# Kernel optimization log

Measured on AMD Instinct MI355X. Metric: run time of the kernel, lower is better.

The kernel has to match this reference:

```python
import jax, jax.numpy as jnp
import numpy as np
from jax import lax

DH = 256   # d_hidden
NL = 8     # number of wavenet cells
K = 3      # kernel_size
DIN = 16   # d_lag + d_cov
DOUT = 1
T, B = 1024, 64


def setup_inputs() -> dict:
    key = jax.random.key(0)
    ks = jax.random.split(key, 20)
    s = 0.05
    inp = {
        "X_emb": jax.random.randint(ks[0], (T, B, 1), 0, 10),
        "X_cov": jax.random.normal(ks[1], (T, B, 8), jnp.float32),
        "X_lag": jax.random.normal(ks[2], (T, B, 8), jnp.float32),
        "y": jax.random.normal(ks[3], (T, B, DOUT), jnp.float32),
        "domain": jax.random.uniform(ks[4], (B, 4), jnp.float32),
        "up_w": jax.random.normal(ks[5], (DIN, DH), jnp.float32) * s,
        "up_b": jnp.zeros((DH,), jnp.float32),
        "conv_dil_w": jax.random.normal(ks[6], (NL, 2 * DH, DH, K), jnp.float32) * s,
        "conv_dil_b": jnp.zeros((NL, 2 * DH), jnp.float32),
        "skip_w": jax.random.normal(ks[7], (NL, 2 * DH, DH), jnp.float32) * s,
        "skip_b": jnp.zeros((NL, 2 * DH), jnp.float32),
        "fc_w": jax.random.normal(ks[8], (DH, DH), jnp.float32) * s,
        "fc_b": jnp.zeros((DH,), jnp.float32),
        "loc_w": jax.random.normal(ks[9], (DH, DOUT), jnp.float32) * s,
        "loc_b": jnp.zeros((DOUT,), jnp.float32),
        "scale_w": jax.random.normal(ks[10], (DH, DOUT), jnp.float32) * s,
        "scale_b": jnp.zeros((DOUT,), jnp.float32),
        "d_outputseqlen": 24,
    }
    return inp


def _causal_conv(h, w, b, dil):
    # h: [B, C, T], w: [O, C, K] -> causal (left-padded) dilated conv
    pad = (w.shape[-1] - 1) * dil
    y = lax.conv_general_dilated(h, w, window_strides=(1,), padding=[(pad, 0)],
                                 rhs_dilation=(dil,),
                                 dimension_numbers=("NCH", "OIH", "NCH"))
    return y + b[None, :, None]


def _forward(X_cov, X_lag, y, up_w, up_b, conv_dil_w, conv_dil_b,
             skip_w, skip_b, fc_w, fc_b, loc_w, loc_b, scale_w, scale_b,
             d_outputseqlen):
    t = X_lag.shape[0]
    h = jnp.concatenate([X_lag, X_cov[:t]], axis=-1) @ up_w + up_b  # [T,B,DH]
    h = jnp.transpose(h, (1, 2, 0))  # [B, DH, T]
    skip = jnp.zeros_like(h)
    for i in range(NL):
        fg = _causal_conv(h, conv_dil_w[i], conv_dil_b[i], 2 ** i)  # [B,2DH,T]
        f, g = jnp.split(fg, 2, axis=1)
        gated = jnp.tanh(f) * jax.nn.sigmoid(g)  # [B,DH,T]
        hs = jnp.einsum("oc,bct->bot", skip_w[i], gated) + skip_b[i][None, :, None]
        h_next, skip_next = jnp.split(hs, 2, axis=1)
        h = h + h_next
        skip = skip + skip_next
    feat = jnp.transpose(skip, (2, 0, 1))  # [T,B,DH]
    ff = jax.nn.relu(feat @ fc_w + fc_b)
    tail = ff[-d_outputseqlen:]
    loc = tail @ loc_w + loc_b
    scale = jax.nn.softplus(tail @ scale_w + scale_b) + 1e-6
    yt = y[-d_outputseqlen:]
    log_prob = (-0.5 * ((yt - loc) / scale) ** 2
                - jnp.log(scale) - 0.5 * np.log(2.0 * np.pi))
    loss_y = -jnp.mean(log_prob)
    total_loss = loss_y  # loss_d forced to 0 in the original forward
    return total_loss, loss_y, loc, scale


def reference(X_emb, X_cov, X_lag, y, domain, up_w, up_b, conv_dil_w,
              conv_dil_b, skip_w, skip_b, fc_w, fc_b, loc_w, loc_b,
              scale_w, scale_b, d_outputseqlen):
    # X_emb and domain are unused with d_emb=[] and loss_d hard-set to 0.
    return _forward(X_cov, X_lag, y, up_w, up_b, conv_dil_w, conv_dil_b,
                    skip_w, skip_b, fc_w, fc_b, loc_w, loc_b,
                    scale_w, scale_b, d_outputseqlen)
```

## Files before the change

kernel.cpp:

```cpp
#include <hip/hip_runtime.h>
#include <math.h>

static constexpr int TT = 1024, BB = 64, DHID = 256, NLAY = 8, OSL = 24;
static constexpr int T0H = 192, THN = 832;
static constexpr int T0G = 256, TGN = 768;

typedef __attribute__((ext_vector_type(8))) short short8;
typedef __attribute__((ext_vector_type(4))) float f32x4;
typedef unsigned short u16;
typedef __attribute__((ext_vector_type(4))) unsigned short u16x4;
typedef unsigned int u32;

__device__ __forceinline__ u16 f2bf(float x) {
  u32 u = __float_as_uint(x);
  return (u16)((u + 0x7fffu + ((u >> 16) & 1u)) >> 16);
}
__device__ __forceinline__ float bf2f(u16 v) {
  return __uint_as_float((u32)v << 16);
}

__global__ __launch_bounds__(256) void wprep(
    const float* __restrict__ cw, const float* __restrict__ sw,
    u16* __restrict__ wP, u16* __restrict__ swH, u16* __restrict__ swG)
{
  const int stride = gridDim.x * 256;
  for (int i = blockIdx.x * 256 + threadIdx.x; i < NLAY * 3 * 8 * 2 * 4 * 2048; i += stride) {
    const int e = i & 7, row = (i >> 3) & 255;
    int q = i >> 11;
    const int p = q & 3; q >>= 2;
    const int cs = q & 1; q >>= 1;
    const int kc = q & 7; q >>= 3;
    const int tap = q % 3, l = q / 3;
    const int o = (row < 128) ? (cs * 128 + row) : (256 + cs * 128 + (row - 128));
    const int c = kc * 32 + p * 8 + e;
    wP[i] = f2bf(cw[((size_t)(l * 512 + o) * 256 + c) * 3 + tap]);
  }
  for (int i = blockIdx.x * 256 + threadIdx.x; i < NLAY * 8 * 4 * 2048; i += stride) {
    const int e = i & 7, o = (i >> 3) & 255, p = (i >> 11) & 3, kc = (i >> 13) & 7, l = i >> 16;
    const int c = kc * 32 + p * 8 + e;
    swH[i] = f2bf(sw[(size_t)(l * 512 + o) * 256 + c]);
    swG[i] = f2bf(sw[(size_t)(l * 512 + 256 + o) * 256 + c]);
  }
}

__global__ __launch_bounds__(256) void up_kernel(
    const float* __restrict__ xlag, const float* __restrict__ xcov,
    const float* __restrict__ upw, const float* __restrict__ upb,
    u16* __restrict__ hb0)
{
  const int b  = blockIdx.y;
  const int t0 = T0H + blockIdx.x * 16;
  __shared__ float xs[16][17];
  {
    const int tl = threadIdx.x >> 4;
    const int j  = threadIdx.x & 15;
    const size_t base = ((size_t)(t0 + tl) * BB + b) * 8;
    xs[tl][j] = (j < 8) ? xlag[base + j] : xcov[base + (j - 8)];
  }
  __syncthreads();
  const int c = threadIdx.x;
  float uw[16];
#pragma unroll
  for (int j = 0; j < 16; ++j) uw[j] = upw[j * DHID + c];
  const float bias = upb[c];
#pragma unroll
  for (int tl = 0; tl < 16; ++tl) {
    float acc = bias;
#pragma unroll
    for (int j = 0; j < 16; ++j) acc = fmaf(xs[tl][j], uw[j], acc);
    hb0[(((size_t)b * 32 + (c >> 3)) * THN + (t0 + tl - T0H)) * 8 + (c & 7)] = f2bf(acc);
  }
}

template <int DIL>
__global__ __launch_bounds__(1024) void conv_gate(
    const u16* __restrict__ hbin, const u16* __restrict__ wPl,
    const float* __restrict__ cb, u16* __restrict__ gbuf,
    u16* __restrict__ g15l, const int tile0)
{
  __shared__ u16 AB[2][16384];
  const int tid = threadIdx.x, w = tid >> 6, lane = tid & 63;
  const int l16 = lane & 15, quad = lane >> 4;
  const int mw = w & 3, nw = w >> 2;
  const int tile = tile0 + (int)(blockIdx.x >> 4);
  const int b0 = (blockIdx.x & 15) * 4;
  const int cs = blockIdx.y;
  const int t0 = tile * 64;

  const int ctb = tid >> 8, pb = (tid >> 6) & 3, tlb = tid & 63;

  const u16* wBase = wPl + (size_t)cs * 8192 + tid * 8;
  const u16* hBase = hbin + (((size_t)(b0 + ctb) * 32 + pb) * THN + (t0 - T0H + tlb)) * 8;

  auto loadA = [&](int step) -> short8 {
    return *(const short8*)(wBase + (size_t)step * 16384);
  };
  auto loadB = [&](int step) -> short8 {
    const int tap = step >> 3, kc = step & 7;
    const int sh = (2 - tap) * DIL;
    return *(const short8*)(hBase + ((size_t)kc * 4 * THN - sh) * 8);
  };

  f32x4 acc[4][4];
  const f32x4 zero = {0.f, 0.f, 0.f, 0.f};
#pragma unroll
  for (int m = 0; m < 4; ++m)
#pragma unroll
    for (int j = 0; j < 4; ++j) acc[m][j] = zero;

  short8 vaN, vbN, vaF, vbF;
  {
    short8 va = loadA(0);
    short8 vb = loadB(0);
    *(short8*)&AB[0][(size_t)tid * 8] = va;
    *(short8*)&AB[0][8192 + (size_t)tid * 8] = vb;
    vaN = loadA(1);
    vbN = loadB(1);
  }
  __syncthreads();

#pragma unroll
  for (int step = 0; step < 24; ++step) {
    const int n2 = step + 2;
    if (n2 < 24) {
      vaF = loadA(n2);
      vbF = loadB(n2);
    }
    const u16* A = AB[step & 1];
    const u16* B = AB[step & 1] + 8192;
    short8 bfr[4];
#pragma unroll
    for (int j = 0; j < 4; ++j)
      bfr[j] = *(const short8*)&B[(nw * 256 + quad * 64 + 16 * j + l16) * 8];
#pragma unroll
    for (int m = 0; m < 4; ++m) {
      const int row = (m < 2) ? (mw * 32 + 16 * m) : (128 + mw * 32 + 16 * (m - 2));
      const short8 a = *(const short8*)&A[(quad * 256 + row + l16) * 8];
#pragma unroll
      for (int j = 0; j < 4; ++j)
        acc[m][j] = __builtin_amdgcn_mfma_f32_16x16x32_bf16(a, bfr[j], acc[m][j], 0, 0, 0);
    }
    const int ns = step + 1;
    if (ns < 24) {
      *(short8*)&AB[ns & 1][(size_t)tid * 8] = vaN;
      *(short8*)&AB[ns & 1][8192 + (size_t)tid * 8] = vbN;
    }
    vaN = vaF; vbN = vbF;
    __syncthreads();
  }

  u16* gT = (u16*)AB;
#pragma unroll
  for (int m = 0; m < 2; ++m) {
    const int c4 = mw * 32 + 16 * m + quad * 4;
    const int cpl = c4 >> 3;
#pragma unroll
    for (int j = 0; j < 4; ++j) {
      const int tl = 16 * j + l16;
      u16x4 pk;
#pragma unroll
      for (int r = 0; r < 4; ++r) {
        const float f = acc[m][j][r]     + cb[cs * 128 + c4 + r];
        const float g = acc[m + 2][j][r] + cb[256 + cs * 128 + c4 + r];
        const float th = 2.f / (1.f + __expf(-2.f * f)) - 1.f;
        const float sg = 1.f / (1.f + __expf(-g));
        pk[r] = f2bf(th * sg);
      }
      *(u16x4*)&gT[((nw * 16 + cpl) * 64 + tl) * 8 + (quad & 1) * 4] = pk;
    }
  }
  __syncthreads();
#pragma unroll
  for (int k = 0; k < 4; ++k) {
    const int slot = k * 1024 + tid;
    const int ct = slot >> 10, cpl = (slot >> 6) & 15, tl = slot & 63;
    const short8 v = *(const short8*)&gT[slot * 8];
    const int b = b0 + ct, cpg = cs * 16 + cpl;
    *(short8*)&gbuf[(((size_t)b * 32 + cpg) * TGN + (t0 + tl - T0G)) * 8] = v;
    if (tile == 15)
      *(short8*)&g15l[(((size_t)b * 32 + cpg) * 64 + tl) * 8] = v;
  }
}

__global__ __launch_bounds__(1024) void skip_h(
    const u16* __restrict__ gbuf, const u16* __restrict__ swHl,
    const float* __restrict__ sb, const u16* __restrict__ hbin,
    u16* __restrict__ hbout, const int tile0)
{
  __shared__ u16 AB[2][16384];
  const int tid = threadIdx.x, w = tid >> 6, lane = tid & 63;
  const int l16 = lane & 15, quad = lane >> 4;
  const int mw = w & 3, nw = w >> 2;
  const int tile = tile0 + (int)(blockIdx.x >> 4);
  const int b0 = (blockIdx.x & 15) * 4;
  const int t0 = tile * 64;

  const int ctb = tid >> 8, pb = (tid >> 6) & 3, tlb = tid & 63;

  const u16* aBase = swHl + tid * 8;
  const u16* bBase = gbuf + (((size_t)(b0 + ctb) * 32 + pb) * TGN + (t0 - T0G + tlb)) * 8;

  auto loadA = [&](int kc) -> short8 {
    return *(const short8*)(aBase + (size_t)kc * 8192);
  };
  auto loadB = [&](int kc) -> short8 {
    return *(const short8*)(bBase + (size_t)kc * 4 * TGN * 8);
  };

  f32x4 acc[4][4];
  const f32x4 zero = {0.f, 0.f, 0.f, 0.f};
#pragma unroll
  for (int m = 0; m < 4; ++m)
#pragma unroll
    for (int j = 0; j < 4; ++j) acc[m][j] = zero;

  short8 vaN, vbN, vaF, vbF;
  {
    short8 va = loadA(0);
    short8 vb = loadB(0);
    *(short8*)&AB[0][(size_t)tid * 8] = va;
    *(short8*)&AB[0][8192 + (size_t)tid * 8] = vb;
    vaN = loadA(1);
    vbN = loadB(1);
  }
  __syncthreads();

#pragma unroll
  for (int step = 0; step < 8; ++step) {
    const int n2 = step + 2;
    if (n2 < 8) { vaF = loadA(n2); vbF = loadB(n2); }
    const u16* A = AB[step & 1];
    const u16* B = AB[step & 1] + 8192;
    short8 bfr[4];
#pragma unroll
    for (int j = 0; j < 4; ++j)
      bfr[j] = *(const short8*)&B[(nw * 256 + quad * 64 + 16 * j + l16) * 8];
#pragma unroll
    for (int m = 0; m < 4; ++m) {
      const short8 a = *(const short8*)&A[(quad * 256 + mw * 64 + 16 * m + l16) * 8];
#pragma unroll
      for (int j = 0; j < 4; ++j)
        acc[m][j] = __builtin_amdgcn_mfma_f32_16x16x32_bf16(a, bfr[j], acc[m][j], 0, 0, 0);
    }
    const int ns = step + 1;
    if (ns < 8) {
      *(short8*)&AB[ns & 1][(size_t)tid * 8] = vaN;
      *(short8*)&AB[ns & 1][8192 + (size_t)tid * 8] = vbN;
    }
    vaN = vaF; vbN = vbF;
    __syncthreads();
  }

  float* fT = (float*)AB;
  for (int ctr = 0; ctr < 4; ++ctr) {
    __syncthreads();
    if (nw == ctr) {
#pragma unroll
      for (int m = 0; m < 4; ++m) {
        const int c4 = mw * 64 + 16 * m + quad * 4;
#pragma unroll
        for (int j = 0; j < 4; ++j) {
          const int tl = 16 * j + l16;
          f32x4 v;
#pragma unroll
          for (int r = 0; r < 4; ++r) v[r] = acc[m][j][r] + sb[c4 + r];
          *(f32x4*)&fT[((c4 >> 3) * 64 + tl) * 8 + (quad & 1) * 4] = v;
        }
      }
    }
    __syncthreads();
    const int b = b0 + ctr;
#pragma unroll
    for (int k = 0; k < 2; ++k) {
      const int slot = k * 1024 + tid;
      const int cpl = slot >> 6, tl = slot & 63;
      const size_t idx = (((size_t)b * 32 + cpl) * THN + (t0 - T0H + tl)) * 8;
      const short8 hv = *(const short8*)&hbin[idx];
      short8 ov;
#pragma unroll
      for (int e = 0; e < 8; ++e)
        ov[e] = (short)f2bf(bf2f((u16)hv[e]) + fT[slot * 8 + e]);
      *(short8*)&hbout[idx] = ov;
    }
  }
}

__global__ __launch_bounds__(512) void skip_g(
    const u16* __restrict__ g15, const u16* __restrict__ swG,
    float* __restrict__ gpart)
{
  __shared__ u16 AB[2][9216];
  const int tid = threadIdx.x, w = tid >> 6, lane = tid & 63;
  const int l16 = lane & 15, quad = lane >> 4;
  const int b = blockIdx.x, l = blockIdx.y;

  const u16* aBase = swG + (size_t)l * 65536 + tid * 8;
  const int pB = tid >> 5, tlB = tid & 31;
  const u16* bBase = g15 + ((((size_t)l * 64 + b) * 32 + pB) * 64 + 32 + tlB) * 8;

  auto loadA = [&](int kc, int q) -> short8 {
    return *(const short8*)(aBase + (size_t)kc * 8192 + q * 4096);
  };
  auto loadB = [&](int kc) -> short8 {
    return *(const short8*)(bBase + (size_t)kc * 4 * 64 * 8);
  };

  f32x4 acc[2][2];
  const f32x4 zero = {0.f, 0.f, 0.f, 0.f};
#pragma unroll
  for (int m = 0; m < 2; ++m)
#pragma unroll
    for (int j = 0; j < 2; ++j) acc[m][j] = zero;

  short8 a0N, a1N, vbN, a0F, a1F, vbF;
  {
    short8 a0 = loadA(0, 0), a1 = loadA(0, 1);
    *(short8*)&AB[0][(size_t)tid * 8] = a0;
    *(short8*)&AB[0][(size_t)(512 + tid) * 8] = a1;
    if (tid < 128) {
      short8 vb = loadB(0);
      *(short8*)&AB[0][8192 + (size_t)tid * 8] = vb;
    }
    a0N = loadA(1, 0); a1N = loadA(1, 1);
    if (tid < 128) vbN = loadB(1);
  }
  __syncthreads();

#pragma unroll
  for (int step = 0; step < 8; ++step) {
    const int n2 = step + 2;
    if (n2 < 8) {
      a0F = loadA(n2, 0); a1F = loadA(n2, 1);
      if (tid < 128) vbF = loadB(n2);
    }
    const u16* A = AB[step & 1];
    const u16* B = AB[step & 1] + 8192;
    short8 bfr[2];
#pragma unroll
    for (int j = 0; j < 2; ++j)
      bfr[j] = *(const short8*)&B[(quad * 32 + 16 * j + l16) * 8];
#pragma unroll
    for (int m = 0; m < 2; ++m) {
      const short8 a = *(const short8*)&A[(quad * 256 + w * 32 + 16 * m + l16) * 8];
#pragma unroll
      for (int j = 0; j < 2; ++j)
        acc[m][j] = __builtin_amdgcn_mfma_f32_16x16x32_bf16(a, bfr[j], acc[m][j], 0, 0, 0);
    }
    const int ns = step + 1;
    if (ns < 8) {
      *(short8*)&AB[ns & 1][(size_t)tid * 8] = a0N;
      *(short8*)&AB[ns & 1][(size_t)(512 + tid) * 8] = a1N;
      if (tid < 128) *(short8*)&AB[ns & 1][8192 + (size_t)tid * 8] = vbN;
    }
    a0N = a0F; a1N = a1F; vbN = vbF;
    __syncthreads();
  }
#pragma unroll
  for (int m = 0; m < 2; ++m)
#pragma unroll
    for (int j = 0; j < 2; ++j)
#pragma unroll
      for (int r = 0; r < 4; ++r) {
        const int c = w * 32 + 16 * m + quad * 4 + r;
        gpart[(((size_t)l * 64 + b) * 256 + c) * 32 + 16 * j + l16] = acc[m][j][r];
      }
}

__global__ __launch_bounds__(256) void head_kernel(
    const float* __restrict__ gpart, const float* __restrict__ skip_b,
    const float* __restrict__ fcw, const float* __restrict__ fcb,
    const float* __restrict__ locw, const float* __restrict__ locb,
    const float* __restrict__ scw, const float* __restrict__ scb,
    float* __restrict__ out)
{
  const int tt = blockIdx.x;
  const int b  = blockIdx.y;
  const int c  = threadIdx.x;
  __shared__ float xs[DHID];
  float s = 0.f;
#pragma unroll
  for (int l = 0; l < NLAY; ++l) {
    s += skip_b[l * 512 + 256 + c];
    s += gpart[(((size_t)l * 64 + b) * 256 + c) * 32 + (8 + tt)];
  }
  xs[c] = s;
  __syncthreads();
  float acc = fcb[c];
#pragma unroll 8
  for (int j = 0; j < DHID; ++j) acc = fmaf(xs[j], fcw[j * DHID + c], acc);
  const float ff = fmaxf(acc, 0.f);
  float pl = ff * locw[c];
  float ps = ff * scw[c];
#pragma unroll
  for (int off = 32; off > 0; off >>= 1) {
    pl += __shfl_down(pl, off);
    ps += __shfl_down(ps, off);
  }
  __shared__ float rl[4], rs[4];
  const int wid = threadIdx.x >> 6, lane = threadIdx.x & 63;
  if (lane == 0) { rl[wid] = pl; rs[wid] = ps; }
  __syncthreads();
  if (threadIdx.x == 0) {
    const float loc = rl[0] + rl[1] + rl[2] + rl[3] + locb[0];
    const float x   = rs[0] + rs[1] + rs[2] + rs[3] + scb[0];
    const float sp  = (x > 0.f) ? (x + log1pf(expf(-x))) : log1pf(expf(x));
    out[2 + tt * BB + b]            = loc;
    out[2 + OSL * BB + tt * BB + b] = sp + 1e-6f;
  }
}

__global__ __launch_bounds__(256) void loss_kernel(
    const float* __restrict__ y, float* __restrict__ out)
{
  float s = 0.f;
  for (int i = threadIdx.x; i < OSL * BB; i += 256) {
    const int tt = i >> 6, b = i & 63;
    const float loc = out[2 + i];
    const float sc  = out[2 + OSL * BB + i];
    const float yt  = y[(size_t)(TT - OSL + tt) * BB + b];
    const float z   = (yt - loc) / sc;
    s += -0.5f * z * z - logf(sc) - 0.9189385332046727f;
  }
#pragma unroll
  for (int off = 32; off > 0; off >>= 1) s += __shfl_down(s, off);
  __shared__ float r[4];
  if ((threadIdx.x & 63) == 0) r[threadIdx.x >> 6] = s;
  __syncthreads();
  if (threadIdx.x == 0) {
    const float loss = -(r[0] + r[1] + r[2] + r[3]) / (float)(OSL * BB);
    out[0] = loss;
    out[1] = loss;
  }
}

extern "C" void kernel_launch(void* const* d_in, const int* in_sizes, int n_in,
                              void* d_out, int out_size, void* d_ws, size_t ws_size,
                              hipStream_t stream) {
  (void)in_sizes; (void)n_in; (void)out_size; (void)ws_size;
  const float* X_cov  = (const float*)d_in[1];
  const float* X_lag  = (const float*)d_in[2];
  const float* y      = (const float*)d_in[3];
  const float* up_w   = (const float*)d_in[5];
  const float* up_b   = (const float*)d_in[6];
  const float* conv_w = (const float*)d_in[7];
  const float* conv_b = (const float*)d_in[8];
  const float* skip_w = (const float*)d_in[9];
  const float* skip_b = (const float*)d_in[10];
  const float* fc_w   = (const float*)d_in[11];
  const float* fc_b   = (const float*)d_in[12];
  const float* loc_w  = (const float*)d_in[13];
  const float* loc_b  = (const float*)d_in[14];
  const float* sc_w   = (const float*)d_in[15];
  const float* sc_b   = (const float*)d_in[16];

  char* wsb = (char*)d_ws;
  u16*   hb0   = (u16*)(wsb + 0);
  u16*   hb1   = (u16*)(wsb + 27262976);
  u16*   gbuf  = (u16*)(wsb + 54525952);
  u16*   g15   = (u16*)(wsb + 79691776);
  u16*   wP    = (u16*)(wsb + 96468992);
  u16*   swH   = (u16*)(wsb + 102760448);
  u16*   swG   = (u16*)(wsb + 103809024);
  float* gpart = (float*)(wsb + 104857600);

  wprep<<<1024, 256, 0, stream>>>(conv_w, skip_w, wP, swH, swG);
  up_kernel<<<dim3(52, BB), 256, 0, stream>>>(X_lag, X_cov, up_w, up_b, hb0);

  static const int Ptab[NLAY] = {4, 5, 6, 7, 8, 9, 11, 15};
  u16* hin = hb0;
  u16* hout = hb1;
  for (int i = 0; i < NLAY; ++i) {
    const int ntiles = 16 - Ptab[i];
    const dim3 cg(ntiles * 16, 2);
    const u16* wPl = wP + (size_t)i * 393216;
    const float* cbl = conv_b + i * 512;
    u16* g15l = g15 + (size_t)i * 1048576;
    switch (i) {
      case 0: conv_gate<1>  <<<cg, 1024, 0, stream>>>(hin, wPl, cbl, gbuf, g15l, Ptab[i]); break;
      case 1: conv_gate<2>  <<<cg, 1024, 0, stream>>>(hin, wPl, cbl, gbuf, g15l, Ptab[i]); break;
      case 2: conv_gate<4>  <<<cg, 1024, 0, stream>>>(hin, wPl, cbl, gbuf, g15l, Ptab[i]); break;
      case 3: conv_gate<8>  <<<cg, 1024, 0, stream>>>(hin, wPl, cbl, gbuf, g15l, Ptab[i]); break;
      case 4: conv_gate<16> <<<cg, 1024, 0, stream>>>(hin, wPl, cbl, gbuf, g15l, Ptab[i]); break;
      case 5: conv_gate<32> <<<cg, 1024, 0, stream>>>(hin, wPl, cbl, gbuf, g15l, Ptab[i]); break;
      case 6: conv_gate<64> <<<cg, 1024, 0, stream>>>(hin, wPl, cbl, gbuf, g15l, Ptab[i]); break;
      case 7: conv_gate<128><<<cg, 1024, 0, stream>>>(hin, wPl, cbl, gbuf, g15l, Ptab[i]); break;
    }
    skip_h<<<dim3(ntiles * 16), 1024, 0, stream>>>(
        gbuf, swH + (size_t)i * 65536, skip_b + i * 512, hin, hout, Ptab[i]);
    u16* tmp = hin; hin = hout; hout = tmp;
  }

  skip_g<<<dim3(64, 8), 512, 0, stream>>>(g15, swG, gpart);
  head_kernel<<<dim3(OSL, BB), 256, 0, stream>>>(
      gpart, skip_b, fc_w, fc_b, loc_w, loc_b, sc_w, sc_b, (float*)d_out);
  loss_kernel<<<1, 256, 0, stream>>>(y, (float*)d_out);
}
```

Measured before the change: 685.4 us.

## Halve block size to 512 threads, de-template dilation, skip last layer's h update

Conv_gate and skip_h now run 512-thread blocks that each cover two batch elements instead of four, with smaller shared buffers and launch bounds asking for 4 blocks per CU. The A-operand tile is loaded as two halves per thread, and the prefetch is shortened from two steps ahead to one. The dilation becomes a runtime argument instead of a template parameter, and the main loops are no longer fully unrolled. The final layer's skip_h launch is dropped, since its h output is never read. The aim is more resident blocks and finer grids for better latency hiding and load balance, at the cost of shallower prefetch and possibly less-optimised non-unrolled loops.

```diff
diff --git a/kernel.cpp b/kernel.cpp
--- a/kernel.cpp
+++ b/kernel.cpp
@@ -72,18 +72,17 @@
   }
 }
 
-template <int DIL>
-__global__ __launch_bounds__(1024) void conv_gate(
+__global__ __launch_bounds__(512, 4) void conv_gate(
     const u16* __restrict__ hbin, const u16* __restrict__ wPl,
     const float* __restrict__ cb, u16* __restrict__ gbuf,
-    u16* __restrict__ g15l, const int tile0)
-{
-  __shared__ u16 AB[2][16384];
+    u16* __restrict__ g15l, const int dil, const int tile0)
+{
+  __shared__ u16 AB[2][12288];
   const int tid = threadIdx.x, w = tid >> 6, lane = tid & 63;
   const int l16 = lane & 15, quad = lane >> 4;
   const int mw = w & 3, nw = w >> 2;
-  const int tile = tile0 + (int)(blockIdx.x >> 4);
-  const int b0 = (blockIdx.x & 15) * 4;
+  const int tile = tile0 + (int)(blockIdx.x >> 5);
+  const int b0 = (blockIdx.x & 31) * 2;
   const int cs = blockIdx.y;
   const int t0 = tile * 64;
 
@@ -92,13 +91,16 @@
   const u16* wBase = wPl + (size_t)cs * 8192 + tid * 8;
   const u16* hBase = hbin + (((size_t)(b0 + ctb) * 32 + pb) * THN + (t0 - T0H + tlb)) * 8;
 
-  auto loadA = [&](int step) -> short8 {
+  auto loadA0 = [&](int step) -> short8 {
     return *(const short8*)(wBase + (size_t)step * 16384);
+  };
+  auto loadA1 = [&](int step) -> short8 {
+    return *(const short8*)(wBase + (size_t)step * 16384 + 4096);
   };
   auto loadB = [&](int step) -> short8 {
     const int tap = step >> 3, kc = step & 7;
-    const int sh = (2 - tap) * DIL;
-    return *(const short8*)(hBase + ((size_t)kc * 4 * THN - sh) * 8);
+    const int sh = (2 - tap) * dil;
+    return *(const short8*)(hBase + ((size_t)(kc * 4) * THN - sh) * 8);
   };
 
   f32x4 acc[4][4];
@@ -108,23 +110,23 @@
 #pragma unroll
     for (int j = 0; j < 4; ++j) acc[m][j] = zero;
 
-  short8 vaN, vbN, vaF, vbF;
+  short8 vbN, vbF;
   {
-    short8 va = loadA(0);
-    short8 vb = loadB(0);
-    *(short8*)&AB[0][(size_t)tid * 8] = va;
-    *(short8*)&AB[0][8192 + (size_t)tid * 8] = vb;
-    vaN = loadA(1);
+    short8 a0 = loadA0(0), a1 = loadA1(0);
+    short8 b  = loadB(0);
+    *(short8*)&AB[0][(size_t)tid * 8] = a0;
+    *(short8*)&AB[0][(size_t)(512 + tid) * 8] = a1;
+    *(short8*)&AB[0][8192 + (size_t)tid * 8] = b;
     vbN = loadB(1);
   }
   __syncthreads();
 
-#pragma unroll
   for (int step = 0; step < 24; ++step) {
-    const int n2 = step + 2;
-    if (n2 < 24) {
-      vaF = loadA(n2);
-      vbF = loadB(n2);
+    const int ns = step + 1;
+    short8 vaN0, vaN1;
+    if (ns < 24) {
+      vaN0 = loadA0(ns); vaN1 = loadA1(ns);
+      if (ns + 1 < 24) vbF = loadB(ns + 1);
     }
     const u16* A = AB[step & 1];
     const u16* B = AB[step & 1] + 8192;
@@ -140,12 +142,12 @@
       for (int j = 0; j < 4; ++j)
         acc[m][j] = __builtin_amdgcn_mfma_f32_16x16x32_bf16(a, bfr[j], acc[m][j], 0, 0, 0);
     }
-    const int ns = step + 1;
     if (ns < 24) {
-      *(short8*)&AB[ns & 1][(size_t)tid * 8] = vaN;
+      *(short8*)&AB[ns & 1][(size_t)tid * 8] = vaN0;
+      *(short8*)&AB[ns & 1][(size_t)(512 + tid) * 8] = vaN1;
       *(short8*)&AB[ns & 1][8192 + (size_t)tid * 8] = vbN;
-    }
-    vaN = vaF; vbN = vbF;
+      vbN = vbF;
+    }
     __syncthreads();
   }
 
@@ -172,7 +174,7 @@
   __syncthreads();
 #pragma unroll
   for (int k = 0; k < 4; ++k) {
-    const int slot = k * 1024 + tid;
+    const int slot = k * 512 + tid;
     const int ct = slot >> 10, cpl = (slot >> 6) & 15, tl = slot & 63;
     const short8 v = *(const short8*)&gT[slot * 8];
     const int b = b0 + ct, cpg = cs * 16 + cpl;
@@ -182,17 +184,17 @@
   }
 }
 
-__global__ __launch_bounds__(1024) void skip_h(
+__global__ __launch_bounds__(512, 4) void skip_h(
     const u16* __restrict__ gbuf, const u16* __restrict__ swHl,
     const float* __restrict__ sb, const u16* __restrict__ hbin,
     u16* __restrict__ hbout, const int tile0)
 {
-  __shared__ u16 AB[2][16384];
+  __shared__ u16 AB[2][12288];
   const int tid = threadIdx.x, w = tid >> 6, lane = tid & 63;
   const int l16 = lane & 15, quad = lane >> 4;
   const int mw = w & 3, nw = w >> 2;
-  const int tile = tile0 + (int)(blockIdx.x >> 4);
-  const int b0 = (blockIdx.x & 15) * 4;
+  const int tile = tile0 + (int)(blockIdx.x >> 5);
+  const int b0 = (blockIdx.x & 31) * 2;
   const int t0 = tile * 64;
 
   const int ctb = tid >> 8, pb = (tid >> 6) & 3, tlb = tid & 63;
@@ -200,8 +202,11 @@
   const u16* aBase = swHl + tid * 8;
   const u16* bBase = gbuf + (((size_t)(b0 + ctb) * 32 + pb) * TGN + (t0 - T0G + tlb)) * 8;
 
-  auto loadA = [&](int kc) -> short8 {
+  auto loadA0 = [&](int kc) -> short8 {
     return *(const short8*)(aBase + (size_t)kc * 8192);
+  };
+  auto loadA1 = [&](int kc) -> short8 {
+    return *(const short8*)(aBase + (size_t)kc * 8192 + 4096);
   };
   auto loadB = [&](int kc) -> short8 {
     return *(const short8*)(bBase + (size_t)kc * 4 * TGN * 8);
@@ -214,21 +219,24 @@
 #pragma unroll
     for (int j = 0; j < 4; ++j) acc[m][j] = zero;
 
-  short8 vaN, vbN, vaF, vbF;
+  short8 vbN, vbF;
   {
-    short8 va = loadA(0);
-    short8 vb = loadB(0);
-    *(short8*)&AB[0][(size_t)tid * 8] = va;
-    *(short8*)&AB[0][8192 + (size_t)tid * 8] = vb;
-    vaN = loadA(1);
+    short8 a0 = loadA0(0), a1 = loadA1(0);
+    short8 b  = loadB(0);
+    *(short8*)&AB[0][(size_t)tid * 8] = a0;
+    *(short8*)&AB[0][(size_t)(512 + tid) * 8] = a1;
+    *(short8*)&AB[0][8192 + (size_t)tid * 8] = b;
     vbN = loadB(1);
   }
   __syncthreads();
 
-#pragma unroll
   for (int step = 0; step < 8; ++step) {
-    const int n2 = step + 2;
-    if (n2 < 8) { vaF = loadA(n2); vbF = loadB(n2); }
+    const int ns = step + 1;
+    short8 vaN0, vaN1;
+    if (ns < 8) {
+      vaN0 = loadA0(ns); vaN1 = loadA1(ns);
+      if (ns + 1 < 8) vbF = loadB(ns + 1);
+    }
     const u16* A = AB[step & 1];
     const u16* B = AB[step & 1] + 8192;
     short8 bfr[4];
@@ -242,45 +250,48 @@
       for (int j = 0; j < 4; ++j)
         acc[m][j] = __builtin_amdgcn_mfma_f32_16x16x32_bf16(a, bfr[j], acc[m][j], 0, 0, 0);
     }
-    const int ns = step + 1;
     if (ns < 8) {
-      *(short8*)&AB[ns & 1][(size_t)tid * 8] = vaN;
+      *(short8*)&AB[ns & 1][(size_t)tid * 8] = vaN0;
+      *(short8*)&AB[ns & 1][(size_t)(512 + tid) * 8] = vaN1;
       *(short8*)&AB[ns & 1][8192 + (size_t)tid * 8] = vbN;
-    }
-    vaN = vaF; vbN = vbF;
+      vbN = vbF;
+    }
     __syncthreads();
   }
 
   float* fT = (float*)AB;
-  for (int ctr = 0; ctr < 4; ++ctr) {
-    __syncthreads();
-    if (nw == ctr) {
-#pragma unroll
-      for (int m = 0; m < 4; ++m) {
-        const int c4 = mw * 64 + 16 * m + quad * 4;
-#pragma unroll
-        for (int j = 0; j < 4; ++j) {
-          const int tl = 16 * j + l16;
-          f32x4 v;
-#pragma unroll
-          for (int r = 0; r < 4; ++r) v[r] = acc[m][j][r] + sb[c4 + r];
-          *(f32x4*)&fT[((c4 >> 3) * 64 + tl) * 8 + (quad & 1) * 4] = v;
+  for (int ctr = 0; ctr < 2; ++ctr) {
+    for (int hh = 0; hh < 2; ++hh) {
+      __syncthreads();
+      if (nw == ctr && (mw >> 1) == hh) {
+#pragma unroll
+        for (int m = 0; m < 4; ++m) {
+          const int c4 = mw * 64 + 16 * m + quad * 4;
+          const int rl = c4 & 127;
+#pragma unroll
+          for (int j = 0; j < 4; ++j) {
+            const int tl = 16 * j + l16;
+            f32x4 v;
+#pragma unroll
+            for (int r = 0; r < 4; ++r) v[r] = acc[m][j][r] + sb[c4 + r];
+            *(f32x4*)&fT[((rl >> 3) * 64 + tl) * 8 + (quad & 1) * 4] = v;
+          }
         }
       }
-    }
-    __syncthreads();
-    const int b = b0 + ctr;
-#pragma unroll
-    for (int k = 0; k < 2; ++k) {
-      const int slot = k * 1024 + tid;
-      const int cpl = slot >> 6, tl = slot & 63;
-      const size_t idx = (((size_t)b * 32 + cpl) * THN + (t0 - T0H + tl)) * 8;
-      const short8 hv = *(const short8*)&hbin[idx];
-      short8 ov;
-#pragma unroll
-      for (int e = 0; e < 8; ++e)
-        ov[e] = (short)f2bf(bf2f((u16)hv[e]) + fT[slot * 8 + e]);
-      *(short8*)&hbout[idx] = ov;
+      __syncthreads();
+      const int b = b0 + ctr;
+#pragma unroll
+      for (int k = 0; k < 2; ++k) {
+        const int slot = k * 512 + tid;
+        const int cpl = slot >> 6, tl = slot & 63;
+        const size_t idx = (((size_t)b * 32 + hh * 16 + cpl) * THN + (t0 - T0H + tl)) * 8;
+        const short8 hv = *(const short8*)&hbin[idx];
+        short8 ov;
+#pragma unroll
+        for (int e = 0; e < 8; ++e)
+          ov[e] = (short)f2bf(bf2f((u16)hv[e]) + fT[slot * 8 + e]);
+        *(short8*)&hbout[idx] = ov;
+      }
     }
   }
 }
@@ -326,7 +337,6 @@
   }
   __syncthreads();
 
-#pragma unroll
   for (int step = 0; step < 8; ++step) {
     const int n2 = step + 2;
     if (n2 < 8) {
@@ -471,23 +481,14 @@
   u16* hout = hb1;
   for (int i = 0; i < NLAY; ++i) {
     const int ntiles = 16 - Ptab[i];
-    const dim3 cg(ntiles * 16, 2);
-    const u16* wPl = wP + (size_t)i * 393216;
-    const float* cbl = conv_b + i * 512;
-    u16* g15l = g15 + (size_t)i * 1048576;
-    switch (i) {
-      case 0: conv_gate<1>  <<<cg, 1024, 0, stream>>>(hin, wPl, cbl, gbuf, g15l, Ptab[i]); break;
-      case 1: conv_gate<2>  <<<cg, 1024, 0, stream>>>(hin, wPl, cbl, gbuf, g15l, Ptab[i]); break;
-      case 2: conv_gate<4>  <<<cg, 1024, 0, stream>>>(hin, wPl, cbl, gbuf, g15l, Ptab[i]); break;
-      case 3: conv_gate<8>  <<<cg, 1024, 0, stream>>>(hin, wPl, cbl, gbuf, g15l, Ptab[i]); break;
-      case 4: conv_gate<16> <<<cg, 1024, 0, stream>>>(hin, wPl, cbl, gbuf, g15l, Ptab[i]); break;
-      case 5: conv_gate<32> <<<cg, 1024, 0, stream>>>(hin, wPl, cbl, gbuf, g15l, Ptab[i]); break;
-      case 6: conv_gate<64> <<<cg, 1024, 0, stream>>>(hin, wPl, cbl, gbuf, g15l, Ptab[i]); break;
-      case 7: conv_gate<128><<<cg, 1024, 0, stream>>>(hin, wPl, cbl, gbuf, g15l, Ptab[i]); break;
-    }
-    skip_h<<<dim3(ntiles * 16), 1024, 0, stream>>>(
-        gbuf, swH + (size_t)i * 65536, skip_b + i * 512, hin, hout, Ptab[i]);
-    u16* tmp = hin; hin = hout; hout = tmp;
+    conv_gate<<<dim3(ntiles * 32, 2), 512, 0, stream>>>(
+        hin, wP + (size_t)i * 393216, conv_b + i * 512, gbuf,
+        g15 + (size_t)i * 1048576, 1 << i, Ptab[i]);
+    if (i < NLAY - 1) {
+      skip_h<<<dim3(ntiles * 32), 512, 0, stream>>>(
+          gbuf, swH + (size_t)i * 65536, skip_b + i * 512, hin, hout, Ptab[i]);
+      u16* tmp = hin; hin = hout; hout = tmp;
+    }
   }
 
   skip_g<<<dim3(64, 8), 512, 0, stream>>>(g15, swG, gpart);
```

After: 598.4 us. 12.7% less time.
